# Performance work log

Measured on AMD Instinct MI355X. Metric: run time of the kernel, lower is better.

The kernel has to match this reference:

```python
import jax, jax.numpy as jnp
import numpy as np

V, D, S, B = 50000, 256, 128, 64

def setup_inputs() -> dict:
    key = jax.random.key(0)
    k0, k1, k2, k3, k4 = jax.random.split(key, 5)
    return {
        "questions": jax.random.randint(k0, (B, S), 0, V),
        "q_position": jax.random.uniform(k1, (B, S), dtype=jnp.float32),
        "word_emb": jax.random.normal(k2, (V, D), dtype=jnp.float32) * 0.02,
        "cmp_emb": jax.random.normal(k3, (V, D), dtype=jnp.float32) * 0.02,
        "weighted_q": jax.random.normal(k4, (S,), dtype=jnp.float32),
    }

def reference(questions, q_position, word_emb, cmp_emb, weighted_q):
    # concat_embedding (dropout is identity in eval / p=0)
    R = word_emb[questions]                              # [B,S,D] real part
    I = cmp_emb[questions] * q_position[..., None]       # [B,S,D] imag part, scaled by position
    w = weighted_q                                       # [S] (original shape (1,S,1,1) squeezed)
    # density_matrix: weighted sum over seq of per-token complex outer products.
    # torch builds real = r r^T + i i^T, imag = i r^T - r i^T per token, then
    # weighted-sums over S; fused here as weighted batched GEMMs V^T diag(w) V.
    real = jnp.einsum('bsd,s,bse->bde', R, w, R) + jnp.einsum('bsd,s,bse->bde', I, w, I)
    imag = jnp.einsum('bsd,s,bse->bde', I, w, R) - jnp.einsum('bsd,s,bse->bde', R, w, I)
    return real, imag
```

## Files before the change

kernel.cpp:

```cpp
#include <hip/hip_runtime.h>
#include <stdint.h>
#include <stddef.h>

#define DD 256
#define SS 128
#define BB 64

typedef __bf16 bf16x8 __attribute__((ext_vector_type(8)));
typedef float  f32x4  __attribute__((ext_vector_type(4)));
typedef unsigned int u32x4 __attribute__((ext_vector_type(4)));
typedef unsigned int u32x2 __attribute__((ext_vector_type(2)));

#define LSTRIDE 136
#define BUFSZ   (128 * LSTRIDE)

__device__ __forceinline__ unsigned f2bf(float x) {
    union { float f; unsigned u; } v; v.f = x;
    unsigned r = v.u + 0x7FFFu + ((v.u >> 16) & 1u);
    return r >> 16;
}

__device__ __forceinline__ void issue_loads(const float* __restrict__ src, const int4 q,
                                            int cb, int cg, f32x4 v[2][4]) {
    #pragma unroll
    for (int it = 0; it < 2; ++it) {
        const int cl = cb + 4 * (cg + 16 * it);
        v[it][0] = *(const f32x4*)(src + (size_t)q.x * DD + cl);
        v[it][1] = *(const f32x4*)(src + (size_t)q.y * DD + cl);
        v[it][2] = *(const f32x4*)(src + (size_t)q.z * DD + cl);
        v[it][3] = *(const f32x4*)(src + (size_t)q.w * DD + cl);
    }
}

__device__ __forceinline__ void cvt_write(unsigned short* __restrict__ dst, const f32x4 scl,
                                          int s0, int cg, f32x4 v[2][4]) {
    #pragma unroll
    for (int it = 0; it < 2; ++it) {
        const int cll = 4 * (cg + 16 * it);
        f32x4 a = v[it][0] * scl[0];
        f32x4 b = v[it][1] * scl[1];
        f32x4 c = v[it][2] * scl[2];
        f32x4 d = v[it][3] * scl[3];
        #pragma unroll
        for (int j = 0; j < 4; ++j) {
            u32x2 pk;
            pk.x = f2bf(a[j]) | (f2bf(b[j]) << 16);
            pk.y = f2bf(c[j]) | (f2bf(d[j]) << 16);
            *(u32x2*)&dst[(cll + j) * LSTRIDE + s0] = pk;
        }
    }
}

template <int KS, int DI0>
__device__ __forceinline__ void mfma_part(const unsigned short* __restrict__ s,
                                          int wr, int wc, int m, int kg,
                                          f32x4 accR[4][4], f32x4 accI[4][4]) {
    const int k0 = KS * 32 + kg * 8;
    const unsigned short* pRw = s;
    const unsigned short* pIw = s + BUFSZ;
    const unsigned short* pR  = s + 2 * BUFSZ;
    const unsigned short* pI  = s + 3 * BUFSZ;
    bf16x8 bR[4], bI[4];
    #pragma unroll
    for (int t = 0; t < 4; ++t) {
        const int rb = (wc * 64 + t * 16 + m) * LSTRIDE + k0;
        bR[t] = *(const bf16x8*)(pR + rb);
        bI[t] = *(const bf16x8*)(pI + rb);
    }
    #pragma unroll
    for (int dd = 0; dd < 2; ++dd) {
        const int di = DI0 + dd;
        const int ra = (wr * 64 + di * 16 + m) * LSTRIDE + k0;
        bf16x8 aR = *(const bf16x8*)(pRw + ra);
        bf16x8 aI = *(const bf16x8*)(pIw + ra);
        u32x4 raw = __builtin_bit_cast(u32x4, aR) ^ 0x80008000u;
        bf16x8 aRn = __builtin_bit_cast(bf16x8, raw);
        #pragma unroll
        for (int ei = 0; ei < 4; ++ei) {
            accR[di][ei] = __builtin_amdgcn_mfma_f32_16x16x32_bf16(aR,  bR[ei], accR[di][ei], 0, 0, 0);
            accR[di][ei] = __builtin_amdgcn_mfma_f32_16x16x32_bf16(aI,  bI[ei], accR[di][ei], 0, 0, 0);
            accI[di][ei] = __builtin_amdgcn_mfma_f32_16x16x32_bf16(aI,  bR[ei], accI[di][ei], 0, 0, 0);
            accI[di][ei] = __builtin_amdgcn_mfma_f32_16x16x32_bf16(aRn, bI[ei], accI[di][ei], 0, 0, 0);
        }
    }
}

__global__ __launch_bounds__(256, 1)
void cmp_density_kernel(const int*   __restrict__ questions,
                        const float* __restrict__ q_position,
                        const float* __restrict__ word_emb,
                        const float* __restrict__ cmp_emb,
                        const float* __restrict__ weighted_q,
                        float*       __restrict__ out)
{
    __shared__ __align__(16) unsigned short s16[4 * BUFSZ];

    const int tid = threadIdx.x;
    const int bx  = blockIdx.x;
    const int b   = bx >> 2;
    const int td  = (bx >> 1) & 1;
    const int te  = bx & 1;

    const int sg = tid & 15;
    const int cg = tid >> 4;
    const int lane = tid & 63;
    const int wv   = tid >> 6;
    const int wr   = wv >> 1;
    const int wc   = wv & 1;
    const int m    = lane & 15;
    const int kg   = lane >> 4;

    const int4  q0 = *(const int4*)(questions + b * SS + 4 * sg);
    const int4  q1 = *(const int4*)(questions + b * SS + 64 + 4 * sg);
    const f32x4 p0 = *(const f32x4*)(q_position + b * SS + 4 * sg);
    const f32x4 p1 = *(const f32x4*)(q_position + b * SS + 64 + 4 * sg);
    const f32x4 w0 = *(const f32x4*)(weighted_q + 4 * sg);
    const f32x4 w1 = *(const f32x4*)(weighted_q + 64 + 4 * sg);
    const f32x4 ones = {1.f, 1.f, 1.f, 1.f};

    f32x4 vA[2][4], vB[2][4];

    issue_loads(word_emb, q0, td * 128, cg, vA);
    issue_loads(cmp_emb,  q0, td * 128, cg, vB);
    cvt_write(s16 + 0 * BUFSZ, w0,      4 * sg, cg, vA);
    cvt_write(s16 + 1 * BUFSZ, w0 * p0, 4 * sg, cg, vB);
    issue_loads(word_emb, q0, te * 128, cg, vA);
    issue_loads(cmp_emb,  q0, te * 128, cg, vB);
    cvt_write(s16 + 2 * BUFSZ, ones, 4 * sg, cg, vA);
    cvt_write(s16 + 3 * BUFSZ, p0,   4 * sg, cg, vB);
    __syncthreads();

    f32x4 accR[4][4] = {};
    f32x4 accI[4][4] = {};

    issue_loads(word_emb, q1, td * 128, cg, vA);
    mfma_part<0, 0>(s16, wr, wc, m, kg, accR, accI);
    cvt_write(s16 + 0 * BUFSZ, w1, 64 + 4 * sg, cg, vA);
    issue_loads(cmp_emb, q1, td * 128, cg, vB);
    mfma_part<0, 2>(s16, wr, wc, m, kg, accR, accI);
    cvt_write(s16 + 1 * BUFSZ, w1 * p1, 64 + 4 * sg, cg, vB);
    issue_loads(word_emb, q1, te * 128, cg, vA);
    mfma_part<1, 0>(s16, wr, wc, m, kg, accR, accI);
    cvt_write(s16 + 2 * BUFSZ, ones, 64 + 4 * sg, cg, vA);
    issue_loads(cmp_emb, q1, te * 128, cg, vB);
    mfma_part<1, 2>(s16, wr, wc, m, kg, accR, accI);
    cvt_write(s16 + 3 * BUFSZ, p1, 64 + 4 * sg, cg, vB);
    __syncthreads();

    mfma_part<2, 0>(s16, wr, wc, m, kg, accR, accI);
    mfma_part<2, 2>(s16, wr, wc, m, kg, accR, accI);
    mfma_part<3, 0>(s16, wr, wc, m, kg, accR, accI);
    mfma_part<3, 2>(s16, wr, wc, m, kg, accR, accI);

    float* outR = out + (size_t)b * DD * DD;
    float* outI = out + (size_t)BB * DD * DD + (size_t)b * DD * DD;
    const int d0 = td * 128 + wr * 64;
    const int e0 = te * 128 + wc * 64;
    #pragma unroll
    for (int di = 0; di < 4; ++di) {
        #pragma unroll
        for (int ei = 0; ei < 4; ++ei) {
            const int e = e0 + ei * 16 + m;
            #pragma unroll
            for (int r = 0; r < 4; ++r) {
                const int d = d0 + di * 16 + kg * 4 + r;
                outR[d * DD + e] = accR[di][ei][r];
                outI[d * DD + e] = accI[di][ei][r];
            }
        }
    }
}

extern "C" void kernel_launch(void* const* d_in, const int* in_sizes, int n_in,
                              void* d_out, int out_size, void* d_ws, size_t ws_size,
                              hipStream_t stream) {
    const int*   questions  = (const int*)d_in[0];
    const float* q_position = (const float*)d_in[1];
    const float* word_emb   = (const float*)d_in[2];
    const float* cmp_emb    = (const float*)d_in[3];
    const float* weighted_q = (const float*)d_in[4];
    float* out = (float*)d_out;
    (void)in_sizes; (void)n_in; (void)d_ws; (void)ws_size; (void)out_size;

    cmp_density_kernel<<<dim3(BB * 4), dim3(256), 0, stream>>>(
        questions, q_position, word_emb, cmp_emb, weighted_q, out);
}
```

Baseline: 134.9 us.

## Double block to 512 threads, halve per-wave tile, use native bf16 conversion

Doubles the threads per block from 256 to 512 (8 waves). Each wave now computes a 64x32 output tile instead of 64x64, and each thread gathers half as many embedding rows. B fragments are loaded once per k-step and reused across the two DI halves, and the manual round-to-nearest-even bf16 conversion is replaced with the native __bf16 cast. The aim is more latency hiding for the gather loads and lower register pressure, at the cost of more waves sharing the same LDS and more A-fragment reads per output.

```diff
diff --git a/kernel.cpp b/kernel.cpp
--- a/kernel.cpp
+++ b/kernel.cpp
@@ -14,58 +14,54 @@
 #define LSTRIDE 136
 #define BUFSZ   (128 * LSTRIDE)
 
-__device__ __forceinline__ unsigned f2bf(float x) {
-    union { float f; unsigned u; } v; v.f = x;
-    unsigned r = v.u + 0x7FFFu + ((v.u >> 16) & 1u);
-    return r >> 16;
+__device__ __forceinline__ unsigned pk2bf(float x, float y) {
+    __bf16 lo = (__bf16)x;
+    __bf16 hi = (__bf16)y;
+    unsigned short ul = __builtin_bit_cast(unsigned short, lo);
+    unsigned short uh = __builtin_bit_cast(unsigned short, hi);
+    return (unsigned)ul | ((unsigned)uh << 16);
 }
 
 __device__ __forceinline__ void issue_loads(const float* __restrict__ src, const int4 q,
-                                            int cb, int cg, f32x4 v[2][4]) {
-    #pragma unroll
-    for (int it = 0; it < 2; ++it) {
-        const int cl = cb + 4 * (cg + 16 * it);
-        v[it][0] = *(const f32x4*)(src + (size_t)q.x * DD + cl);
-        v[it][1] = *(const f32x4*)(src + (size_t)q.y * DD + cl);
-        v[it][2] = *(const f32x4*)(src + (size_t)q.z * DD + cl);
-        v[it][3] = *(const f32x4*)(src + (size_t)q.w * DD + cl);
-    }
+                                            int cl, f32x4 v[4]) {
+    v[0] = *(const f32x4*)(src + (size_t)q.x * DD + cl);
+    v[1] = *(const f32x4*)(src + (size_t)q.y * DD + cl);
+    v[2] = *(const f32x4*)(src + (size_t)q.z * DD + cl);
+    v[3] = *(const f32x4*)(src + (size_t)q.w * DD + cl);
 }
 
 __device__ __forceinline__ void cvt_write(unsigned short* __restrict__ dst, const f32x4 scl,
-                                          int s0, int cg, f32x4 v[2][4]) {
+                                          int s0, int cll, f32x4 v[4]) {
+    f32x4 a = v[0] * scl[0];
+    f32x4 b = v[1] * scl[1];
+    f32x4 c = v[2] * scl[2];
+    f32x4 d = v[3] * scl[3];
     #pragma unroll
-    for (int it = 0; it < 2; ++it) {
-        const int cll = 4 * (cg + 16 * it);
-        f32x4 a = v[it][0] * scl[0];
-        f32x4 b = v[it][1] * scl[1];
-        f32x4 c = v[it][2] * scl[2];
-        f32x4 d = v[it][3] * scl[3];
-        #pragma unroll
-        for (int j = 0; j < 4; ++j) {
-            u32x2 pk;
-            pk.x = f2bf(a[j]) | (f2bf(b[j]) << 16);
-            pk.y = f2bf(c[j]) | (f2bf(d[j]) << 16);
-            *(u32x2*)&dst[(cll + j) * LSTRIDE + s0] = pk;
-        }
+    for (int j = 0; j < 4; ++j) {
+        u32x2 pk;
+        pk.x = pk2bf(a[j], b[j]);
+        pk.y = pk2bf(c[j], d[j]);
+        *(u32x2*)&dst[(cll + j) * LSTRIDE + s0] = pk;
     }
 }
 
 template <int KS, int DI0>
 __device__ __forceinline__ void mfma_part(const unsigned short* __restrict__ s,
+                                          bf16x8 bR[2], bf16x8 bI[2],
                                           int wr, int wc, int m, int kg,
-                                          f32x4 accR[4][4], f32x4 accI[4][4]) {
+                                          f32x4 accR[4][2], f32x4 accI[4][2]) {
     const int k0 = KS * 32 + kg * 8;
     const unsigned short* pRw = s;
     const unsigned short* pIw = s + BUFSZ;
     const unsigned short* pR  = s + 2 * BUFSZ;
     const unsigned short* pI  = s + 3 * BUFSZ;
-    bf16x8 bR[4], bI[4];
-    #pragma unroll
-    for (int t = 0; t < 4; ++t) {
-        const int rb = (wc * 64 + t * 16 + m) * LSTRIDE + k0;
-        bR[t] = *(const bf16x8*)(pR + rb);
-        bI[t] = *(const bf16x8*)(pI + rb);
+    if (DI0 == 0) {
+        #pragma unroll
+        for (int t = 0; t < 2; ++t) {
+            const int rb = (wc * 32 + t * 16 + m) * LSTRIDE + k0;
+            bR[t] = *(const bf16x8*)(pR + rb);
+            bI[t] = *(const bf16x8*)(pI + rb);
+        }
     }
     #pragma unroll
     for (int dd = 0; dd < 2; ++dd) {
@@ -76,7 +72,7 @@
         u32x4 raw = __builtin_bit_cast(u32x4, aR) ^ 0x80008000u;
         bf16x8 aRn = __builtin_bit_cast(bf16x8, raw);
         #pragma unroll
-        for (int ei = 0; ei < 4; ++ei) {
+        for (int ei = 0; ei < 2; ++ei) {
             accR[di][ei] = __builtin_amdgcn_mfma_f32_16x16x32_bf16(aR,  bR[ei], accR[di][ei], 0, 0, 0);
             accR[di][ei] = __builtin_amdgcn_mfma_f32_16x16x32_bf16(aI,  bI[ei], accR[di][ei], 0, 0, 0);
             accI[di][ei] = __builtin_amdgcn_mfma_f32_16x16x32_bf16(aI,  bR[ei], accI[di][ei], 0, 0, 0);
@@ -85,7 +81,7 @@
     }
 }
 
-__global__ __launch_bounds__(256, 1)
+__global__ __launch_bounds__(512, 2)
 void cmp_density_kernel(const int*   __restrict__ questions,
                         const float* __restrict__ q_position,
                         const float* __restrict__ word_emb,
@@ -101,12 +97,15 @@
     const int td  = (bx >> 1) & 1;
     const int te  = bx & 1;
 
-    const int sg = tid & 15;
-    const int cg = tid >> 4;
+    const int sg  = tid & 15;
+    const int cg  = (tid >> 4) & 15;
+    const int hb  = tid >> 8;
+    const int cll = 4 * (cg + 16 * hb);
+
     const int lane = tid & 63;
     const int wv   = tid >> 6;
-    const int wr   = wv >> 1;
-    const int wc   = wv & 1;
+    const int wr   = wv >> 2;
+    const int wc   = wv & 3;
     const int m    = lane & 15;
     const int kg   = lane >> 4;
 
@@ -117,49 +116,52 @@
     const f32x4 w0 = *(const f32x4*)(weighted_q + 4 * sg);
     const f32x4 w1 = *(const f32x4*)(weighted_q + 64 + 4 * sg);
     const f32x4 ones = {1.f, 1.f, 1.f, 1.f};
+    const f32x4 wp0 = w0 * p0;
+    const f32x4 wp1 = w1 * p1;
 
-    f32x4 vA[2][4], vB[2][4];
+    f32x4 vA[4], vB[4];
 
-    issue_loads(word_emb, q0, td * 128, cg, vA);
-    issue_loads(cmp_emb,  q0, td * 128, cg, vB);
-    cvt_write(s16 + 0 * BUFSZ, w0,      4 * sg, cg, vA);
-    cvt_write(s16 + 1 * BUFSZ, w0 * p0, 4 * sg, cg, vB);
-    issue_loads(word_emb, q0, te * 128, cg, vA);
-    issue_loads(cmp_emb,  q0, te * 128, cg, vB);
-    cvt_write(s16 + 2 * BUFSZ, ones, 4 * sg, cg, vA);
-    cvt_write(s16 + 3 * BUFSZ, p0,   4 * sg, cg, vB);
+    issue_loads(word_emb, q0, td * 128 + cll, vA);
+    issue_loads(cmp_emb,  q0, td * 128 + cll, vB);
+    cvt_write(s16 + 0 * BUFSZ, w0,  4 * sg, cll, vA);
+    cvt_write(s16 + 1 * BUFSZ, wp0, 4 * sg, cll, vB);
+    issue_loads(word_emb, q0, te * 128 + cll, vA);
+    issue_loads(cmp_emb,  q0, te * 128 + cll, vB);
+    cvt_write(s16 + 2 * BUFSZ, ones, 4 * sg, cll, vA);
+    cvt_write(s16 + 3 * BUFSZ, p0,   4 * sg, cll, vB);
     __syncthreads();
 
-    f32x4 accR[4][4] = {};
-    f32x4 accI[4][4] = {};
+    f32x4 accR[4][2] = {};
+    f32x4 accI[4][2] = {};
+    bf16x8 bR[2], bI[2];
 
-    issue_loads(word_emb, q1, td * 128, cg, vA);
-    mfma_part<0, 0>(s16, wr, wc, m, kg, accR, accI);
-    cvt_write(s16 + 0 * BUFSZ, w1, 64 + 4 * sg, cg, vA);
-    issue_loads(cmp_emb, q1, td * 128, cg, vB);
-    mfma_part<0, 2>(s16, wr, wc, m, kg, accR, accI);
-    cvt_write(s16 + 1 * BUFSZ, w1 * p1, 64 + 4 * sg, cg, vB);
-    issue_loads(word_emb, q1, te * 128, cg, vA);
-    mfma_part<1, 0>(s16, wr, wc, m, kg, accR, accI);
-    cvt_write(s16 + 2 * BUFSZ, ones, 64 + 4 * sg, cg, vA);
-    issue_loads(cmp_emb, q1, te * 128, cg, vB);
-    mfma_part<1, 2>(s16, wr, wc, m, kg, accR, accI);
-    cvt_write(s16 + 3 * BUFSZ, p1, 64 + 4 * sg, cg, vB);
+    issue_loads(word_emb, q1, td * 128 + cll, vA);
+    mfma_part<0, 0>(s16, bR, bI, wr, wc, m, kg, accR, accI);
+    cvt_write(s16 + 0 * BUFSZ, w1, 64 + 4 * sg, cll, vA);
+    issue_loads(cmp_emb, q1, td * 128 + cll, vB);
+    mfma_part<0, 2>(s16, bR, bI, wr, wc, m, kg, accR, accI);
+    cvt_write(s16 + 1 * BUFSZ, wp1, 64 + 4 * sg, cll, vB);
+    issue_loads(word_emb, q1, te * 128 + cll, vA);
+    mfma_part<1, 0>(s16, bR, bI, wr, wc, m, kg, accR, accI);
+    cvt_write(s16 + 2 * BUFSZ, ones, 64 + 4 * sg, cll, vA);
+    issue_loads(cmp_emb, q1, te * 128 + cll, vB);
+    mfma_part<1, 2>(s16, bR, bI, wr, wc, m, kg, accR, accI);
+    cvt_write(s16 + 3 * BUFSZ, p1, 64 + 4 * sg, cll, vB);
     __syncthreads();
 
-    mfma_part<2, 0>(s16, wr, wc, m, kg, accR, accI);
-    mfma_part<2, 2>(s16, wr, wc, m, kg, accR, accI);
-    mfma_part<3, 0>(s16, wr, wc, m, kg, accR, accI);
-    mfma_part<3, 2>(s16, wr, wc, m, kg, accR, accI);
+    mfma_part<2, 0>(s16, bR, bI, wr, wc, m, kg, accR, accI);
+    mfma_part<2, 2>(s16, bR, bI, wr, wc, m, kg, accR, accI);
+    mfma_part<3, 0>(s16, bR, bI, wr, wc, m, kg, accR, accI);
+    mfma_part<3, 2>(s16, bR, bI, wr, wc, m, kg, accR, accI);
 
     float* outR = out + (size_t)b * DD * DD;
     float* outI = out + (size_t)BB * DD * DD + (size_t)b * DD * DD;
     const int d0 = td * 128 + wr * 64;
-    const int e0 = te * 128 + wc * 64;
+    const int e0 = te * 128 + wc * 32;
     #pragma unroll
     for (int di = 0; di < 4; ++di) {
         #pragma unroll
-        for (int ei = 0; ei < 4; ++ei) {
+        for (int ei = 0; ei < 2; ++ei) {
             const int e = e0 + ei * 16 + m;
             #pragma unroll
             for (int r = 0; r < 4; ++r) {
@@ -182,6 +184,6 @@
     float* out = (float*)d_out;
     (void)in_sizes; (void)n_in; (void)d_ws; (void)ws_size; (void)out_size;
 
-    cmp_density_kernel<<<dim3(BB * 4), dim3(256), 0, stream>>>(
+    cmp_density_kernel<<<dim3(BB * 4), dim3(512), 0, stream>>>(
         questions, q_position, word_emb, cmp_emb, weighted_q, out);
 }
```

After: 134.1 us. No clear change (-0.6%).
